# Performance work log

Hardware: AMD Instinct MI355X
Metric: run time of the kernel (lower is better)

Reference implementation:

```python
import jax, jax.numpy as jnp
import numpy as np
import math

B, I, H = 8192, 1024, 1024

def _uniform(key, shape, lo, hi):
    return jax.random.uniform(key, shape, dtype=jnp.float32, minval=lo, maxval=hi)

def setup_inputs() -> dict:
    key = jax.random.key(0)
    ks = jax.random.split(key, 14)
    bound = math.sqrt(1.0 / H)
    lo, hi = -bound, bound
    x = jax.random.normal(ks[0], (B, I), dtype=jnp.float32)
    hid = jax.random.normal(ks[1], (B, H), dtype=jnp.float32)
    # stacked params for gates [r, z, n]
    wx = jnp.stack([_uniform(ks[2 + i], (I, H), lo, hi) for i in range(3)])   # [3, I, H]
    wh = jnp.stack([_uniform(ks[5 + i], (H, H), lo, hi) for i in range(3)])   # [3, H, H]
    bx = jnp.stack([_uniform(ks[8 + i], (H,), lo, hi) for i in range(3)])     # [3, H]
    bh = jnp.stack([_uniform(ks[11 + i], (H,), lo, hi) for i in range(3)])    # [3, H]
    return {"x": x, "hid": hid, "wx": wx, "wh": wh, "bx": bx, "bh": bh}

def reference(x, hid, wx, wh, bx, bh):
    # Fused gate projections: one big matmul per source instead of 3 small ones.
    gx = jnp.einsum('bi,gih->bgh', x, wx) + bx[None]        # [B, 3, H]
    gh = jnp.einsum('bh,ghk->bgk', hid, wh) + bh[None]      # [B, 3, H]
    r = jax.nn.sigmoid(gx[:, 0] + gh[:, 0])
    z = jax.nn.sigmoid(gx[:, 1] + gh[:, 1])
    n = jnp.tanh(gx[:, 2] + r * gh[:, 2])
    next_hid = (1.0 - z) * n + z * hid
    return next_hid
```

## Files before the change

### kernel.cpp

```cpp
#include <hip/hip_runtime.h>
#include <hip/hip_bf16.h>

typedef __hip_bfloat16 bf16;
typedef unsigned short u16;
typedef __attribute__((ext_vector_type(8))) short bf16x8;
typedef __attribute__((ext_vector_type(4))) float f32x4;
typedef __attribute__((ext_vector_type(8))) unsigned short u16x8;

#define KD 1024
#define HD 1024
#define BSZ 8192
#define BM 256
#define BN 64
#define BK 32
#define NT (KD / BK)

#define WS_XB 12582912
#define WS_HB 29360128
#define WS_NEED 46137344ULL

__device__ __forceinline__ u16 f2b(float f) {
    return __builtin_bit_cast(u16, __float2bfloat16(f));
}

__device__ __forceinline__ void gload16(const void* g, u16* smem, int lds_byte_off) {
    __builtin_amdgcn_global_load_lds(
        (const __attribute__((address_space(1))) void*)g,
        (__attribute__((address_space(3))) void*)((char*)smem + lds_byte_off),
        16, 0, 0);
}

__global__ __launch_bounds__(256) void convert_xh(
    const float* __restrict__ x, const float* __restrict__ h,
    u16* __restrict__ xb, u16* __restrict__ hb)
{
    size_t off = ((size_t)blockIdx.x * 256 + threadIdx.x) * 8;
    float4 a0 = *(const float4*)(x + off);
    float4 a1 = *(const float4*)(x + off + 4);
    float4 b0 = *(const float4*)(h + off);
    float4 b1 = *(const float4*)(h + off + 4);
    u16x8 vx, vh;
    vx[0]=f2b(a0.x); vx[1]=f2b(a0.y); vx[2]=f2b(a0.z); vx[3]=f2b(a0.w);
    vx[4]=f2b(a1.x); vx[5]=f2b(a1.y); vx[6]=f2b(a1.z); vx[7]=f2b(a1.w);
    vh[0]=f2b(b0.x); vh[1]=f2b(b0.y); vh[2]=f2b(b0.z); vh[3]=f2b(b0.w);
    vh[4]=f2b(b1.x); vh[5]=f2b(b1.y); vh[6]=f2b(b1.z); vh[7]=f2b(b1.w);
    *(u16x8*)(xb + off) = vx;
    *(u16x8*)(hb + off) = vh;
}

__global__ __launch_bounds__(256) void transpose_w(
    const float* __restrict__ wx, const float* __restrict__ wh, u16* __restrict__ wt)
{
    __shared__ float tile[64 * 69];
    const int b = blockIdx.x;
    const int t = threadIdx.x;
    const int g  = b >> 8;
    const int rm = b & 255;
    const int r0 = (rm >> 4) * 64;
    const int c0 = (rm & 15) * 64;
    const float* src = (g < 3) ? (wx + (size_t)g * KD * HD)
                               : (wh + (size_t)(g - 3) * KD * HD);
    u16* dst = wt + (size_t)g * KD * HD;

    #pragma unroll
    for (int ps = 0; ps < 4; ps++) {
        int idx = ps * 256 + t;
        int row = idx >> 4;
        int c4  = (idx & 15) * 4;
        float4 v = *(const float4*)(src + (size_t)(r0 + row) * HD + c0 + c4);
        *(float4*)&tile[row * 69 + c4] = v;
    }
    __syncthreads();
    const int n = t >> 2;
    #pragma unroll
    for (int p = 0; p < 2; p++) {
        int k0 = (t & 3) * 8 + p * 32;
        u16x8 v;
        #pragma unroll
        for (int e = 0; e < 8; e++)
            v[e] = f2b(tile[(k0 + e) * 69 + n]);
        *(u16x8*)(dst + (size_t)(c0 + n) * KD + r0 + k0) = v;
    }
}

__device__ __forceinline__ void gru_epilogue(
    f32x4 (&acc)[4][4][2], const float* __restrict__ bxf, const float* __restrict__ bhf,
    const float* __restrict__ hidf, float* __restrict__ outf,
    int m0, int n0, int wm, int wn, int quad, int c16)
{
    float bR[2], bZ[2], bXN[2], bHN[2];
    #pragma unroll
    for (int j = 0; j < 2; j++) {
        int col = n0 + wn * 32 + j * 16 + c16;
        bR[j]  = bxf[col]          + bhf[col];
        bZ[j]  = bxf[HD + col]     + bhf[HD + col];
        bXN[j] = bxf[2 * HD + col];
        bHN[j] = bhf[2 * HD + col];
    }
    #pragma unroll
    for (int i = 0; i < 4; i++)
        #pragma unroll
        for (int j = 0; j < 2; j++) {
            int col = n0 + wn * 32 + j * 16 + c16;
            #pragma unroll
            for (int r = 0; r < 4; r++) {
                int row = m0 + wm * 64 + i * 16 + quad * 4 + r;
                size_t idx = (size_t)row * HD + col;
                float vr = acc[0][i][j][r] + bR[j];
                vr = 1.f / (1.f + __expf(-vr));
                float vz = acc[1][i][j][r] + bZ[j];
                vz = 1.f / (1.f + __expf(-vz));
                float vn = (acc[2][i][j][r] + bXN[j]) + vr * (acc[3][i][j][r] + bHN[j]);
                float e2 = __expf(2.f * vn);
                vn = 1.f - 2.f / (e2 + 1.f);
                float o = (1.f - vz) * vn + vz * hidf[idx];
                outf[idx] = o;
            }
        }
}

__global__ __launch_bounds__(512, 2) void gru_fused_fast(
    const u16* __restrict__ xb, const u16* __restrict__ hb,
    const u16* __restrict__ wt,
    const float* __restrict__ bxf, const float* __restrict__ bhf,
    const float* __restrict__ hidf, float* __restrict__ outf)
{
    __shared__ u16 smem[57344];
    const int t    = threadIdx.x;
    const int lane = t & 63;
    const int w    = t >> 6;
    const int wm   = w >> 1, wn = w & 1;
    const int quad = lane >> 4;
    const int c16  = lane & 15;
    const int lin  = blockIdx.x;
    const int nblk = (lin & 7) * 2 + ((lin >> 3) & 1);
    const int mblk = lin >> 4;
    const int m0   = mblk * BM;
    const int n0   = nblk * BN;

    const int row4 = t >> 2;
    const int e8s  = ((t & 3) ^ ((t >> 3) & 3)) * 8;
    const u16* gxa = xb + (size_t)(m0 + row4) * KD + e8s;
    const u16* gxb = gxa + (size_t)128 * KD;
    const u16* gha = hb + (size_t)(m0 + row4) * KD + e8s;
    const u16* ghb = gha + (size_t)128 * KD;
    const int wrow = (t >> 2) & 63;
    const int wsel = (t >> 8) & 1;
    const u16* gw0 = wt + (size_t)(0 + wsel) * KD * HD + (size_t)(n0 + wrow) * KD + e8s;
    const u16* gw1 = wt + (size_t)(2 + wsel) * KD * HD + (size_t)(n0 + wrow) * KD + e8s;
    const u16* gw2 = wt + (size_t)(4 + wsel) * KD * HD + (size_t)(n0 + wrow) * KD + e8s;
    const int ldsl = w * 1024;

    f32x4 acc[4][4][2];
    #pragma unroll
    for (int a = 0; a < 4; a++)
        #pragma unroll
        for (int i = 0; i < 4; i++)
            #pragma unroll
            for (int j = 0; j < 2; j++)
                acc[a][i][j] = (f32x4){0.f, 0.f, 0.f, 0.f};

    auto stage = [&](int bufb) {
        gload16(gxa, smem, bufb + 0     + ldsl);
        gload16(gxb, smem, bufb + 8192  + ldsl);
        gload16(gha, smem, bufb + 16384 + ldsl);
        gload16(ghb, smem, bufb + 24576 + ldsl);
        gload16(gw0, smem, bufb + 32768 + ldsl);
        gload16(gw1, smem, bufb + 40960 + ldsl);
        gload16(gw2, smem, bufb + 49152 + ldsl);
        gxa += BK; gxb += BK; gha += BK; ghb += BK;
        gw0 += BK; gw1 += BK; gw2 += BK;
    };

    auto compute = [&](const u16* sm) {
        bf16x8 ax[4], ah[4];
        #pragma unroll
        for (int i = 0; i < 4; i++) {
            int ml = wm * 64 + i * 16 + c16;
            int sl = (quad ^ ((ml >> 1) & 3)) * 8;
            ax[i] = *(const bf16x8*)&sm[ml * 32 + sl];
            ah[i] = *(const bf16x8*)&sm[8192 + ml * 32 + sl];
        }
        #pragma unroll
        for (int p = 0; p < 3; p++) {
            bf16x8 bwx[2], bwh[2];
            #pragma unroll
            for (int j = 0; j < 2; j++) {
                int nl = wn * 32 + j * 16 + c16;
                int sl = (quad ^ ((nl >> 1) & 3)) * 8;
                bwx[j] = *(const bf16x8*)&sm[16384 + p * 2048       + nl * 32 + sl];
                bwh[j] = *(const bf16x8*)&sm[16384 + (p + 3) * 2048 + nl * 32 + sl];
            }
            #pragma unroll
            for (int i = 0; i < 4; i++)
                #pragma unroll
                for (int j = 0; j < 2; j++) {
                    if (p < 2) {
                        acc[p][i][j] = __builtin_amdgcn_mfma_f32_16x16x32_bf16(ax[i], bwx[j], acc[p][i][j], 0, 0, 0);
                        acc[p][i][j] = __builtin_amdgcn_mfma_f32_16x16x32_bf16(ah[i], bwh[j], acc[p][i][j], 0, 0, 0);
                    } else {
                        acc[2][i][j] = __builtin_amdgcn_mfma_f32_16x16x32_bf16(ax[i], bwx[j], acc[2][i][j], 0, 0, 0);
                        acc[3][i][j] = __builtin_amdgcn_mfma_f32_16x16x32_bf16(ah[i], bwh[j], acc[3][i][j], 0, 0, 0);
                    }
                }
        }
    };

    stage(0);
    __syncthreads();

    for (int tt = 0; tt < NT - 1; ++tt) {
        stage(((tt + 1) & 1) * 57344);
        compute(smem + (tt & 1) * 28672);
        __syncthreads();
    }
    compute(smem + 28672);

    gru_epilogue(acc, bxf, bhf, hidf, outf, m0, n0, wm, wn, quad, c16);
}

__device__ __forceinline__ void kstep_compute_lds(
    const u16* sm, f32x4 (&acc)[4][4][2], int wm, int wn, int quad, int c16)
{
    bf16x8 ax[4], ah[4];
    #pragma unroll
    for (int i = 0; i < 4; i++) {
        int ml = wm * 64 + i * 16 + c16;
        int sl = (quad ^ ((ml >> 1) & 3)) * 8;
        ax[i] = *(const bf16x8*)&sm[ml * BK + sl];
        ah[i] = *(const bf16x8*)&sm[4096 + ml * BK + sl];
    }
    #pragma unroll
    for (int p = 0; p < 3; p++) {
        bf16x8 bwx[2], bwh[2];
        #pragma unroll
        for (int j = 0; j < 2; j++) {
            int nl = wn * 32 + j * 16 + c16;
            int sl = (quad ^ ((nl >> 1) & 3)) * 8;
            bwx[j] = *(const bf16x8*)&sm[8192 + p * 2048       + nl * BK + sl];
            bwh[j] = *(const bf16x8*)&sm[8192 + (p + 3) * 2048 + nl * BK + sl];
        }
        #pragma unroll
        for (int i = 0; i < 4; i++)
            #pragma unroll
            for (int j = 0; j < 2; j++) {
                if (p < 2) {
                    acc[p][i][j] = __builtin_amdgcn_mfma_f32_16x16x32_bf16(ax[i], bwx[j], acc[p][i][j], 0, 0, 0);
                    acc[p][i][j] = __builtin_amdgcn_mfma_f32_16x16x32_bf16(ah[i], bwh[j], acc[p][i][j], 0, 0, 0);
                } else {
                    acc[2][i][j] = __builtin_amdgcn_mfma_f32_16x16x32_bf16(ax[i], bwx[j], acc[2][i][j], 0, 0, 0);
                    acc[3][i][j] = __builtin_amdgcn_mfma_f32_16x16x32_bf16(ah[i], bwh[j], acc[3][i][j], 0, 0, 0);
                }
            }
    }
}

__global__ __launch_bounds__(256, 2) void gru_fused_slow(
    const float* __restrict__ xf, const float* __restrict__ hf,
    const u16* __restrict__ wt,
    const float* __restrict__ bxf, const float* __restrict__ bhf,
    float* __restrict__ outf)
{
    __shared__ u16 smem[20480];
    const int t    = threadIdx.x;
    const int lane = t & 63;
    const int w    = t >> 6;
    const int wm   = w >> 1, wn = w & 1;
    const int quad = lane >> 4;
    const int c16  = lane & 15;
    const int lin  = blockIdx.x;
    const int nblk = (lin & 7) * 2 + ((lin >> 3) & 1);
    const int mblk = lin >> 4;
    const int m0   = mblk * 128;
    const int n0   = nblk * BN;
    const int row4 = t >> 2;
    const int e8s  = ((t & 3) ^ ((t >> 3) & 3)) * 8;
    const u16* gw0 = wt + (size_t)(n0 + row4) * KD + e8s;
    const int ldsl = w * 1024;

    f32x4 acc[4][4][2];
    #pragma unroll
    for (int a = 0; a < 4; a++)
        #pragma unroll
        for (int i = 0; i < 4; i++)
            #pragma unroll
            for (int j = 0; j < 2; j++)
                acc[a][i][j] = (f32x4){0.f, 0.f, 0.f, 0.f};

    for (int k0 = 0; k0 < KD; k0 += BK) {
        #pragma unroll
        for (int g = 0; g < 6; g++)
            gload16(gw0 + (size_t)g * KD * HD, smem, 16384 + g * 4096 + ldsl);
        gw0 += BK;
        #pragma unroll
        for (int s = 0; s < 2; s++) {
            size_t gidx = (size_t)(m0 + s * 64 + row4) * KD + k0 + (t & 3) * 8;
            const float* px = xf + gidx;
            const float* ph = hf + gidx;
            u16x8 vx, vh;
            #pragma unroll
            for (int e = 0; e < 8; e++) { vx[e] = f2b(px[e]); vh[e] = f2b(ph[e]); }
            *(u16x8*)&smem[s * 2048 + row4 * 32 + e8s] = vx;
            *(u16x8*)&smem[4096 + s * 2048 + row4 * 32 + e8s] = vh;
        }
        __syncthreads();
        kstep_compute_lds(smem, acc, wm, wn, quad, c16);
        __syncthreads();
    }

    gru_epilogue(acc, bxf, bhf, hf, outf, m0, n0, wm, wn, quad, c16);
}

extern "C" void kernel_launch(void* const* d_in, const int* in_sizes, int n_in,
                              void* d_out, int out_size, void* d_ws, size_t ws_size,
                              hipStream_t stream) {
    const float* x   = (const float*)d_in[0];
    const float* hid = (const float*)d_in[1];
    const float* wx  = (const float*)d_in[2];
    const float* wh  = (const float*)d_in[3];
    const float* bx  = (const float*)d_in[4];
    const float* bh  = (const float*)d_in[5];
    float* out = (float*)d_out;

    char* ws = (char*)d_ws;
    u16* wt = (u16*)ws;
    u16* xb = (u16*)(ws + WS_XB);
    u16* hb = (u16*)(ws + WS_HB);

    transpose_w<<<1536, 256, 0, stream>>>(wx, wh, wt);

    if (ws_size >= WS_NEED) {
        convert_xh<<<4096, 256, 0, stream>>>(x, hid, xb, hb);
        gru_fused_fast<<<512, 512, 0, stream>>>(xb, hb, wt, bx, bh, hid, out);
    } else {
        gru_fused_slow<<<1024, 256, 0, stream>>>(x, hid, wt, bx, bh, out);
    }
}
```

Measured before the change: 242.4 us.

## Deepen pipeline to triple-buffered activations with interleaved loads, barriers and setprio

Splits staging into separate activation and weight loads. Activations are now triple-buffered and weights double-buffered, in a larger LDS allocation. The K loop is restructured into three gate phases, with global prefetches issued between them, explicit s_waitcnt vmcnt counts, and s_setprio raised around MFMA bursts. The aim is to hide global-load latency behind compute and keep MFMA issue dense across waves. In exchange it adds more barriers per iteration and a bigger LDS footprint (144 KB), which may limit occupancy. Buffer-index and vmcnt accounting is intricate and could hide hazards.

```diff
diff --git a/kernel.cpp b/kernel.cpp
--- a/kernel.cpp
+++ b/kernel.cpp
@@ -125,7 +125,7 @@
     const float* __restrict__ bxf, const float* __restrict__ bhf,
     const float* __restrict__ hidf, float* __restrict__ outf)
 {
-    __shared__ u16 smem[57344];
+    __shared__ u16 smem[73728];
     const int t    = threadIdx.x;
     const int lane = t & 63;
     const int w    = t >> 6;
@@ -144,7 +144,7 @@
     const u16* gxb = gxa + (size_t)128 * KD;
     const u16* gha = hb + (size_t)(m0 + row4) * KD + e8s;
     const u16* ghb = gha + (size_t)128 * KD;
-    const int wrow = (t >> 2) & 63;
+    const int wrow = row4 & 63;
     const int wsel = (t >> 8) & 1;
     const u16* gw0 = wt + (size_t)(0 + wsel) * KD * HD + (size_t)(n0 + wrow) * KD + e8s;
     const u16* gw1 = wt + (size_t)(2 + wsel) * KD * HD + (size_t)(n0 + wrow) * KD + e8s;
@@ -160,61 +160,102 @@
             for (int j = 0; j < 2; j++)
                 acc[a][i][j] = (f32x4){0.f, 0.f, 0.f, 0.f};
 
-    auto stage = [&](int bufb) {
+    auto stage_xh = [&](int bufb) {
         gload16(gxa, smem, bufb + 0     + ldsl);
         gload16(gxb, smem, bufb + 8192  + ldsl);
         gload16(gha, smem, bufb + 16384 + ldsl);
         gload16(ghb, smem, bufb + 24576 + ldsl);
-        gload16(gw0, smem, bufb + 32768 + ldsl);
-        gload16(gw1, smem, bufb + 40960 + ldsl);
-        gload16(gw2, smem, bufb + 49152 + ldsl);
         gxa += BK; gxb += BK; gha += BK; ghb += BK;
+    };
+    auto stage_w = [&](int bufb) {
+        gload16(gw0, smem, bufb + 0     + ldsl);
+        gload16(gw1, smem, bufb + 8192  + ldsl);
+        gload16(gw2, smem, bufb + 16384 + ldsl);
         gw0 += BK; gw1 += BK; gw2 += BK;
     };
 
-    auto compute = [&](const u16* sm) {
+    stage_xh(0);
+    stage_w(98304);
+    stage_xh(32768);
+    asm volatile("s_waitcnt vmcnt(4)" ::: "memory");
+    __builtin_amdgcn_s_barrier();
+
+    for (int tt = 0; tt < NT; ++tt) {
+        const u16* smx = smem + (tt % 3) * 16384;
+        const u16* smw = smem + 49152 + (tt & 1) * 12288;
+
         bf16x8 ax[4], ah[4];
         #pragma unroll
         for (int i = 0; i < 4; i++) {
             int ml = wm * 64 + i * 16 + c16;
             int sl = (quad ^ ((ml >> 1) & 3)) * 8;
-            ax[i] = *(const bf16x8*)&sm[ml * 32 + sl];
-            ah[i] = *(const bf16x8*)&sm[8192 + ml * 32 + sl];
-        }
-        #pragma unroll
-        for (int p = 0; p < 3; p++) {
-            bf16x8 bwx[2], bwh[2];
+            ax[i] = *(const bf16x8*)&smx[ml * 32 + sl];
+            ah[i] = *(const bf16x8*)&smx[8192 + ml * 32 + sl];
+        }
+        bf16x8 b0x[2], b0h[2];
+        #pragma unroll
+        for (int j = 0; j < 2; j++) {
+            int nl = wn * 32 + j * 16 + c16;
+            int sl = (quad ^ ((nl >> 1) & 3)) * 8;
+            b0x[j] = *(const bf16x8*)&smw[0 * 2048 + nl * 32 + sl];
+            b0h[j] = *(const bf16x8*)&smw[3 * 2048 + nl * 32 + sl];
+        }
+        if (tt + 1 < NT) stage_w(98304 + ((tt + 1) & 1) * 24576);
+        __builtin_amdgcn_s_barrier();
+        __builtin_amdgcn_s_setprio(1);
+        #pragma unroll
+        for (int i = 0; i < 4; i++)
             #pragma unroll
             for (int j = 0; j < 2; j++) {
-                int nl = wn * 32 + j * 16 + c16;
-                int sl = (quad ^ ((nl >> 1) & 3)) * 8;
-                bwx[j] = *(const bf16x8*)&sm[16384 + p * 2048       + nl * 32 + sl];
-                bwh[j] = *(const bf16x8*)&sm[16384 + (p + 3) * 2048 + nl * 32 + sl];
-            }
-            #pragma unroll
-            for (int i = 0; i < 4; i++)
-                #pragma unroll
-                for (int j = 0; j < 2; j++) {
-                    if (p < 2) {
-                        acc[p][i][j] = __builtin_amdgcn_mfma_f32_16x16x32_bf16(ax[i], bwx[j], acc[p][i][j], 0, 0, 0);
-                        acc[p][i][j] = __builtin_amdgcn_mfma_f32_16x16x32_bf16(ah[i], bwh[j], acc[p][i][j], 0, 0, 0);
-                    } else {
-                        acc[2][i][j] = __builtin_amdgcn_mfma_f32_16x16x32_bf16(ax[i], bwx[j], acc[2][i][j], 0, 0, 0);
-                        acc[3][i][j] = __builtin_amdgcn_mfma_f32_16x16x32_bf16(ah[i], bwh[j], acc[3][i][j], 0, 0, 0);
-                    }
-                }
-        }
-    };
-
-    stage(0);
-    __syncthreads();
-
-    for (int tt = 0; tt < NT - 1; ++tt) {
-        stage(((tt + 1) & 1) * 57344);
-        compute(smem + (tt & 1) * 28672);
-        __syncthreads();
-    }
-    compute(smem + 28672);
+                acc[0][i][j] = __builtin_amdgcn_mfma_f32_16x16x32_bf16(ax[i], b0x[j], acc[0][i][j], 0, 0, 0);
+                acc[0][i][j] = __builtin_amdgcn_mfma_f32_16x16x32_bf16(ah[i], b0h[j], acc[0][i][j], 0, 0, 0);
+            }
+        __builtin_amdgcn_s_setprio(0);
+        __builtin_amdgcn_s_barrier();
+
+        bf16x8 b1x[2], b1h[2];
+        #pragma unroll
+        for (int j = 0; j < 2; j++) {
+            int nl = wn * 32 + j * 16 + c16;
+            int sl = (quad ^ ((nl >> 1) & 3)) * 8;
+            b1x[j] = *(const bf16x8*)&smw[1 * 2048 + nl * 32 + sl];
+            b1h[j] = *(const bf16x8*)&smw[4 * 2048 + nl * 32 + sl];
+        }
+        if (tt + 2 < NT) stage_xh(((tt + 2) % 3) * 32768);
+        __builtin_amdgcn_s_barrier();
+        __builtin_amdgcn_s_setprio(1);
+        #pragma unroll
+        for (int i = 0; i < 4; i++)
+            #pragma unroll
+            for (int j = 0; j < 2; j++) {
+                acc[1][i][j] = __builtin_amdgcn_mfma_f32_16x16x32_bf16(ax[i], b1x[j], acc[1][i][j], 0, 0, 0);
+                acc[1][i][j] = __builtin_amdgcn_mfma_f32_16x16x32_bf16(ah[i], b1h[j], acc[1][i][j], 0, 0, 0);
+            }
+        __builtin_amdgcn_s_setprio(0);
+        __builtin_amdgcn_s_barrier();
+
+        bf16x8 b2x[2], b2h[2];
+        #pragma unroll
+        for (int j = 0; j < 2; j++) {
+            int nl = wn * 32 + j * 16 + c16;
+            int sl = (quad ^ ((nl >> 1) & 3)) * 8;
+            b2x[j] = *(const bf16x8*)&smw[2 * 2048 + nl * 32 + sl];
+            b2h[j] = *(const bf16x8*)&smw[5 * 2048 + nl * 32 + sl];
+        }
+        __builtin_amdgcn_s_barrier();
+        __builtin_amdgcn_s_setprio(1);
+        #pragma unroll
+        for (int i = 0; i < 4; i++)
+            #pragma unroll
+            for (int j = 0; j < 2; j++) {
+                acc[2][i][j] = __builtin_amdgcn_mfma_f32_16x16x32_bf16(ax[i], b2x[j], acc[2][i][j], 0, 0, 0);
+                acc[3][i][j] = __builtin_amdgcn_mfma_f32_16x16x32_bf16(ah[i], b2h[j], acc[3][i][j], 0, 0, 0);
+            }
+        __builtin_amdgcn_s_setprio(0);
+        if (tt + 2 < NT) { asm volatile("s_waitcnt vmcnt(4)" ::: "memory"); }
+        else             { asm volatile("s_waitcnt vmcnt(0)" ::: "memory"); }
+        __builtin_amdgcn_s_barrier();
+    }
 
     gru_epilogue(acc, bxf, bhf, hidf, outf, m0, n0, wm, wn, quad, c16);
 }
```

After: 241.6 us. About the same (-0.3%).
